# Kernel tuning notes

Measured on AMD Instinct MI355X. Metric: run time of the kernel, lower is better.

## Reference

```python
import jax, jax.numpy as jnp
import numpy as np

N_NODES = 100_000
N_EDGES = 1_600_000
N_GRAPHS = 64
IN_CH = 128
HID = 64
OUT_CH = 2


def setup_inputs() -> dict:
    key = jax.random.key(0)
    ks = jax.random.split(key, 12)

    def lin(k, fan_in, fan_out):
        s = 1.0 / np.sqrt(fan_in)
        return jax.random.uniform(k, (fan_in, fan_out), jnp.float32, -s, s)

    x = jax.random.normal(ks[0], (N_NODES, IN_CH), jnp.float32)
    edge_index = jax.random.randint(ks[1], (2, N_EDGES), 0, N_NODES, jnp.int64)
    batch = jnp.sort(jax.random.randint(ks[2], (N_NODES,), 0, N_GRAPHS, jnp.int64))
    return {
        "x": x,
        "edge_index": edge_index,
        "batch": batch,
        "w_rel0": lin(ks[3], IN_CH, HID),
        "b_rel0": jnp.zeros((HID,), jnp.float32),
        "w_root0": lin(ks[4], IN_CH, HID),
        "w_rel1": lin(ks[5], HID, HID),
        "b_rel1": jnp.zeros((HID,), jnp.float32),
        "w_root1": lin(ks[6], HID, HID),
        "w_rel2": lin(ks[7], HID, HID),
        "b_rel2": jnp.zeros((HID,), jnp.float32),
        "w_root2": lin(ks[8], HID, HID),
        "head_w1": lin(ks[9], HID, HID),
        "head_b1": jnp.zeros((HID,), jnp.float32),
        "head_w2": lin(ks[10], HID, OUT_CH),
        "head_b2": jnp.zeros((OUT_CH,), jnp.float32),
    }


def _graph_conv(x, src, dst, w_rel, b_rel, w_root):
    # PyG GraphConv: out = lin_rel(sum_{j->i} x_j) + lin_root(x_i)
    agg = jax.ops.segment_sum(x[src], dst, num_segments=N_NODES)  # [N, d_in]
    return agg @ w_rel + b_rel + x @ w_root


def reference(x, edge_index, batch, w_rel0, b_rel0, w_root0,
              w_rel1, b_rel1, w_root1, w_rel2, b_rel2, w_root2,
              head_w1, head_b1, head_w2, head_b2):
    src, dst = edge_index[0], edge_index[1]
    h = jax.nn.relu(_graph_conv(x, src, dst, w_rel0, b_rel0, w_root0))
    h = jax.nn.relu(_graph_conv(h, src, dst, w_rel1, b_rel1, w_root1))
    h = jax.nn.relu(_graph_conv(h, src, dst, w_rel2, b_rel2, w_root2))
    # global_mean_pool over graph ids (dropout is identity at inference)
    sums = jax.ops.segment_sum(h, batch, num_segments=N_GRAPHS)          # [G, H]
    cnts = jax.ops.segment_sum(jnp.ones((N_NODES,), h.dtype), batch,
                               num_segments=N_GRAPHS)                    # [G]
    pooled = sums / jnp.maximum(cnts, 1.0)[:, None]
    z = jax.nn.relu(pooled @ head_w1 + head_b1)
    return z @ head_w2 + head_b2
```

## Files before the change

### kernel.cpp

```cpp
#include <hip/hip_runtime.h>
#include <hip/hip_bf16.h>

#define CAP 64
#define KBUCK 391
#define BSHIFT 8
#define BCAP 4608
#define CHUNK_A 2048
#define AITER (CHUNK_A / 256)
#define ASTR 40
#define LDSZ (2 * 128 * ASTR * 2)

typedef __attribute__((ext_vector_type(8))) short short8;
typedef __attribute__((ext_vector_type(4))) float f32x4;

__device__ inline unsigned short bfbits(float f) {
    __hip_bfloat16 b = __float2bfloat16(f);
    unsigned short u;
    __builtin_memcpy(&u, &b, 2);
    return u;
}

__device__ inline uint4 pack8(float4 v0, float4 v1) {
    union { uint4 q; unsigned short s[8]; } pk;
    pk.s[0] = bfbits(v0.x); pk.s[1] = bfbits(v0.y);
    pk.s[2] = bfbits(v0.z); pk.s[3] = bfbits(v0.w);
    pk.s[4] = bfbits(v1.x); pk.s[5] = bfbits(v1.y);
    pk.s[6] = bfbits(v1.z); pk.s[7] = bfbits(v1.w);
    return pk.q;
}

__device__ inline void bucket_body(char* smem, int bb, const int* __restrict__ ei,
                                   int E, int* __restrict__ gcur,
                                   unsigned* __restrict__ bucketed)
{
    int* hist = (int*)smem;
    int* base = hist + KBUCK;
    const int e0 = bb * CHUNK_A;
    const int e1 = min(e0 + CHUNK_A, E);
    for (int i = threadIdx.x; i < KBUCK; i += 256) hist[i] = 0;
    __syncthreads();
    int dreg[AITER];
    #pragma unroll
    for (int it = 0; it < AITER; ++it) {
        int e = e0 + it * 256 + threadIdx.x;
        dreg[it] = (e < e1) ? ei[E + e] : -1;
        if (dreg[it] >= 0) atomicAdd(&hist[dreg[it] >> BSHIFT], 1);
    }
    __syncthreads();
    for (int i = threadIdx.x; i < KBUCK; i += 256) {
        int h = hist[i];
        base[i] = h ? atomicAdd(&gcur[i], h) : 0;
        hist[i] = 0;
    }
    __syncthreads();
    #pragma unroll
    for (int it = 0; it < AITER; ++it) {
        int e = e0 + it * 256 + threadIdx.x;
        if (e < e1) {
            int s = ei[e];
            int d = dreg[it];
            int b = d >> BSHIFT;
            int off = base[b] + atomicAdd(&hist[b], 1);
            if (off < BCAP)
                bucketed[(size_t)b * BCAP + off] = ((unsigned)s << 8) | (unsigned)(d & 255);
        }
    }
}

__global__ __launch_bounds__(256) void build_slots_kernel(
    const unsigned* __restrict__ bucketed, const int* __restrict__ gcur,
    int* __restrict__ cnt, int* __restrict__ slots, int N)
{
    __shared__ int lcnt[256];
    const int b = blockIdx.x;
    const int nb0 = b << BSHIFT;
    lcnt[threadIdx.x] = 0;
    __syncthreads();
    const int count = min(gcur[b], BCAP);
    const unsigned* src = bucketed + (size_t)b * BCAP;
    for (int i = threadIdx.x; i < count; i += 256) {
        unsigned p = src[i];
        int dl = (int)(p & 255u);
        int pos = atomicAdd(&lcnt[dl], 1);
        if (pos < CAP) slots[(size_t)(nb0 + dl) * CAP + pos] = (int)(p >> 8);
    }
    __syncthreads();
    int node = nb0 + threadIdx.x;
    if (node < N) cnt[node] = min(lcnt[threadIdx.x], CAP);
}

__global__ __launch_bounds__(256) void prep_weights_kernel(
    const float* __restrict__ wr0, const float* __restrict__ wt0,
    const float* __restrict__ wr1, const float* __restrict__ wt1,
    const float* __restrict__ wr2, const float* __restrict__ wt2,
    __hip_bfloat16* __restrict__ hi, __hip_bfloat16* __restrict__ lo,
    int* __restrict__ gcur, float* __restrict__ gsum, int* __restrict__ gcnt)
{
    int idx = blockIdx.x * 256 + threadIdx.x;
    if (idx < KBUCK) gcur[idx] = 0;
    if (idx < 64 * 64) gsum[idx] = 0.f;
    if (idx < 64) gcnt[idx] = 0;
    if (idx >= 32768) return;
    const float *wr, *wt;
    int n, k;
    if (idx < 16384)      { wr = wr0; wt = wt0; int r = idx;         n = r >> 7; k = r & 127; }
    else if (idx < 24576) { wr = wr1; wt = wt1; int r = idx - 16384; n = r >> 6; k = r & 63; }
    else                  { wr = wr2; wt = wt2; int r = idx - 24576; n = r >> 6; k = r & 63; }
    float w = (n < 64) ? wr[k * 64 + n] : wt[k * 64 + (n - 64)];
    __hip_bfloat16 h = __float2bfloat16(w);
    hi[idx] = h;
    lo[idx] = __float2bfloat16(w - __bfloat162float(h));
}

__device__ inline void store_cd(f32x4 (&acc)[4][4], int node0, int wm, int wn,
                                int kgrp, int lrow, const float* __restrict__ b_rel,
                                __hip_bfloat16* __restrict__ y,
                                __hip_bfloat16* __restrict__ r, int N)
{
    #pragma unroll
    for (int i = 0; i < 4; ++i) {
        int mbase = node0 + wm * 64 + i * 16 + kgrp * 4;
        #pragma unroll
        for (int j = 0; j < 4; ++j) {
            int n = wn * 64 + j * 16 + lrow;
            #pragma unroll
            for (int v = 0; v < 4; ++v) {
                int m = mbase + v;
                if (m < N) {
                    float val = acc[i][j][v];
                    if (n < 64) y[(size_t)m * 64 + n] = __float2bfloat16(val);
                    else        r[(size_t)m * 64 + (n - 64)] = __float2bfloat16(val + b_rel[n - 64]);
                }
            }
        }
    }
}

__device__ inline void mfma_l0_body(char* smem, int bx, const float* __restrict__ x,
    const __hip_bfloat16* __restrict__ whiT, const __hip_bfloat16* __restrict__ wloT,
    const float* __restrict__ b_rel,
    __hip_bfloat16* __restrict__ y, __hip_bfloat16* __restrict__ r, int N)
{
    __hip_bfloat16* As = (__hip_bfloat16*)smem;
    const int t = threadIdx.x;
    const int lane = t & 63;
    const int wid = t >> 6;
    const int wm = wid >> 1, wn = wid & 1;
    const int node0 = bx * 128;
    const int lrow = lane & 15;
    const int kgrp = lane >> 4;

    int sm[2], sk[2];
    const float* sp[2];
    #pragma unroll
    for (int p = 0; p < 2; ++p) {
        int c = t + p * 256;
        sm[p] = c >> 2;
        sk[p] = (c & 3) * 8;
        int row = node0 + sm[p]; if (row >= N) row = N - 1;
        sp[p] = x + (size_t)row * 128 + sk[p];
    }

    f32x4 acc[4][4];
    #pragma unroll
    for (int i = 0; i < 4; ++i)
        #pragma unroll
        for (int j = 0; j < 4; ++j) acc[i][j] = (f32x4){0.f, 0.f, 0.f, 0.f};

    #pragma unroll
    for (int p = 0; p < 2; ++p) {
        float4 v0 = *(const float4*)(sp[p]);
        float4 v1 = *(const float4*)(sp[p] + 4);
        *(uint4*)&As[sm[p] * ASTR + sk[p]] = pack8(v0, v1);
    }
    __syncthreads();

    #pragma unroll
    for (int ks = 0; ks < 4; ++ks) {
        const int buf  = (ks & 1) * (128 * ASTR);
        const int nbuf = ((ks + 1) & 1) * (128 * ASTR);

        float4 nv0[2], nv1[2];
        if (ks < 3) {
            #pragma unroll
            for (int p = 0; p < 2; ++p) {
                nv0[p] = *(const float4*)(sp[p] + (ks + 1) * 32);
                nv1[p] = *(const float4*)(sp[p] + (ks + 1) * 32 + 4);
            }
        }

        short8 a[4], bh[4], bl[4];
        #pragma unroll
        for (int i = 0; i < 4; ++i)
            a[i] = *(const short8*)&As[buf + (wm * 64 + i * 16 + lrow) * ASTR + kgrp * 8];
        #pragma unroll
        for (int j = 0; j < 4; ++j) {
            int n = wn * 64 + j * 16 + lrow;
            bh[j] = *(const short8*)(whiT + (size_t)n * 128 + ks * 32 + kgrp * 8);
            bl[j] = *(const short8*)(wloT + (size_t)n * 128 + ks * 32 + kgrp * 8);
        }
        #pragma unroll
        for (int i = 0; i < 4; ++i)
            #pragma unroll
            for (int j = 0; j < 4; ++j) {
                acc[i][j] = __builtin_amdgcn_mfma_f32_16x16x32_bf16(a[i], bh[j], acc[i][j], 0, 0, 0);
                acc[i][j] = __builtin_amdgcn_mfma_f32_16x16x32_bf16(a[i], bl[j], acc[i][j], 0, 0, 0);
            }

        if (ks < 3) {
            #pragma unroll
            for (int p = 0; p < 2; ++p)
                *(uint4*)&As[nbuf + sm[p] * ASTR + sk[p]] = pack8(nv0[p], nv1[p]);
        }
        __syncthreads();
    }

    store_cd(acc, node0, wm, wn, kgrp, lrow, b_rel, y, r, N);
}

__global__ __launch_bounds__(256) void fused_l0_kernel(
    const float* __restrict__ x,
    const __hip_bfloat16* __restrict__ whiT, const __hip_bfloat16* __restrict__ wloT,
    const float* __restrict__ b_rel,
    __hip_bfloat16* __restrict__ y, __hip_bfloat16* __restrict__ r, int N,
    int gemm_blocks, const int* __restrict__ ei, int E,
    int* __restrict__ gcur, unsigned* __restrict__ bucketed)
{
    extern __shared__ char smem[];
    if ((int)blockIdx.x < gemm_blocks)
        mfma_l0_body(smem, blockIdx.x, x, whiT, wloT, b_rel, y, r, N);
    else
        bucket_body(smem, blockIdx.x - gemm_blocks, ei, E, gcur, bucketed);
}

template <int DIN>
__global__ __launch_bounds__(256) void mfma_lin_kernel(
    const __hip_bfloat16* __restrict__ feat,
    const __hip_bfloat16* __restrict__ whiT, const __hip_bfloat16* __restrict__ wloT,
    const float* __restrict__ b_rel,
    __hip_bfloat16* __restrict__ y, __hip_bfloat16* __restrict__ r, int N)
{
    const int t = threadIdx.x;
    const int lane = t & 63;
    const int wid = t >> 6;
    const int wm = wid >> 1, wn = wid & 1;
    const int node0 = blockIdx.x * 128;
    const int lrow = lane & 15;
    const int kgrp = lane >> 4;

    f32x4 acc[4][4];
    #pragma unroll
    for (int i = 0; i < 4; ++i)
        #pragma unroll
        for (int j = 0; j < 4; ++j) acc[i][j] = (f32x4){0.f, 0.f, 0.f, 0.f};

    #pragma unroll
    for (int ks = 0; ks < DIN / 32; ++ks) {
        short8 a[4], bh[4], bl[4];
        #pragma unroll
        for (int i = 0; i < 4; ++i) {
            int row = node0 + wm * 64 + i * 16 + lrow;
            if (row >= N) row = N - 1;
            a[i] = *(const short8*)(feat + (size_t)row * DIN + ks * 32 + kgrp * 8);
        }
        #pragma unroll
        for (int j = 0; j < 4; ++j) {
            int n = wn * 64 + j * 16 + lrow;
            bh[j] = *(const short8*)(whiT + (size_t)n * DIN + ks * 32 + kgrp * 8);
            bl[j] = *(const short8*)(wloT + (size_t)n * DIN + ks * 32 + kgrp * 8);
        }
        #pragma unroll
        for (int i = 0; i < 4; ++i)
            #pragma unroll
            for (int j = 0; j < 4; ++j) {
                acc[i][j] = __builtin_amdgcn_mfma_f32_16x16x32_bf16(a[i], bh[j], acc[i][j], 0, 0, 0);
                acc[i][j] = __builtin_amdgcn_mfma_f32_16x16x32_bf16(a[i], bl[j], acc[i][j], 0, 0, 0);
            }
    }

    store_cd(acc, node0, wm, wn, kgrp, lrow, b_rel, y, r, N);
}

__global__ __launch_bounds__(256) void gather_relu_kernel(
    const __hip_bfloat16* __restrict__ y, const int* __restrict__ cnt,
    const int* __restrict__ slots, const __hip_bfloat16* __restrict__ rin,
    __hip_bfloat16* __restrict__ hout, int N)
{
    const int node = blockIdx.x * 8 + (threadIdx.x >> 5);
    if (node >= N) return;
    const int sub = threadIdx.x & 31;
    const int nb = sub >> 3;
    const int ch = (sub & 7) * 8;
    const int deg = cnt[node];
    const int* sl = slots + (size_t)node * CAP;
    const unsigned short* yp = (const unsigned short*)y;

    float a[8], b[8];
    #pragma unroll
    for (int k = 0; k < 8; ++k) { a[k] = 0.f; b[k] = 0.f; }

    #pragma unroll 2
    for (int j = nb; j < deg; j += 8) {
        int n0 = sl[j];
        uint4 v = *(const uint4*)(yp + (size_t)n0 * 64 + ch);
        a[0] += __uint_as_float(v.x << 16); a[1] += __uint_as_float(v.x & 0xffff0000u);
        a[2] += __uint_as_float(v.y << 16); a[3] += __uint_as_float(v.y & 0xffff0000u);
        a[4] += __uint_as_float(v.z << 16); a[5] += __uint_as_float(v.z & 0xffff0000u);
        a[6] += __uint_as_float(v.w << 16); a[7] += __uint_as_float(v.w & 0xffff0000u);
        int j2 = j + 4;
        if (j2 < deg) {
            int n1 = sl[j2];
            uint4 w = *(const uint4*)(yp + (size_t)n1 * 64 + ch);
            b[0] += __uint_as_float(w.x << 16); b[1] += __uint_as_float(w.x & 0xffff0000u);
            b[2] += __uint_as_float(w.y << 16); b[3] += __uint_as_float(w.y & 0xffff0000u);
            b[4] += __uint_as_float(w.z << 16); b[5] += __uint_as_float(w.z & 0xffff0000u);
            b[6] += __uint_as_float(w.w << 16); b[7] += __uint_as_float(w.w & 0xffff0000u);
        }
    }
    #pragma unroll
    for (int k = 0; k < 8; ++k) {
        a[k] += b[k];
        a[k] += __shfl_xor(a[k], 8);
        a[k] += __shfl_xor(a[k], 16);
    }
    if (nb == 0) {
        uint4 rv = *(const uint4*)((const unsigned short*)rin + (size_t)node * 64 + ch);
        float r0 = __uint_as_float(rv.x << 16), r1 = __uint_as_float(rv.x & 0xffff0000u);
        float r2 = __uint_as_float(rv.y << 16), r3 = __uint_as_float(rv.y & 0xffff0000u);
        float r4 = __uint_as_float(rv.z << 16), r5 = __uint_as_float(rv.z & 0xffff0000u);
        float r6 = __uint_as_float(rv.w << 16), r7 = __uint_as_float(rv.w & 0xffff0000u);
        float f0 = fmaxf(r0 + a[0], 0.f), f1 = fmaxf(r1 + a[1], 0.f);
        float f2 = fmaxf(r2 + a[2], 0.f), f3 = fmaxf(r3 + a[3], 0.f);
        float f4 = fmaxf(r4 + a[4], 0.f), f5 = fmaxf(r5 + a[5], 0.f);
        float f6 = fmaxf(r6 + a[6], 0.f), f7 = fmaxf(r7 + a[7], 0.f);
        union { uint4 q; unsigned short s[8]; } pk;
        pk.s[0] = bfbits(f0); pk.s[1] = bfbits(f1); pk.s[2] = bfbits(f2); pk.s[3] = bfbits(f3);
        pk.s[4] = bfbits(f4); pk.s[5] = bfbits(f5); pk.s[6] = bfbits(f6); pk.s[7] = bfbits(f7);
        *(uint4*)((unsigned short*)hout + (size_t)node * 64 + ch) = pk.q;
    }
}

__global__ __launch_bounds__(256) void pool_kernel(
    const __hip_bfloat16* __restrict__ h, const int* __restrict__ batch,
    float* __restrict__ gsum, int* __restrict__ gcnt, int N)
{
    const int CHUNK = 64;
    int wid = (blockIdx.x * 256 + threadIdx.x) >> 6;
    int lane = threadIdx.x & 63;
    int nb = lane >> 3;
    int ch = (lane & 7) * 8;
    int start = wid * CHUNK;
    if (start >= N) return;
    int end = min(start + CHUNK, N);
    const unsigned short* hp = (const unsigned short*)h;

    float a[8];
    #pragma unroll
    for (int k = 0; k < 8; ++k) a[k] = 0.f;
    int runcnt = 0;
    int i = start;
    int gcur = batch[start];

    while (i < end) {
        int idx = i + lane; if (idx > end - 1) idx = end - 1;
        int bl = batch[idx];
        unsigned long long diff = __ballot(bl != gcur && (i + lane) < end);
        int len = diff ? ((int)__ffsll(diff) - 1) : min(64, end - i);
        for (int j = i + nb; j < i + len; j += 8) {
            uint4 v = *(const uint4*)(hp + (size_t)j * 64 + ch);
            a[0] += __uint_as_float(v.x << 16); a[1] += __uint_as_float(v.x & 0xffff0000u);
            a[2] += __uint_as_float(v.y << 16); a[3] += __uint_as_float(v.y & 0xffff0000u);
            a[4] += __uint_as_float(v.z << 16); a[5] += __uint_as_float(v.z & 0xffff0000u);
            a[6] += __uint_as_float(v.w << 16); a[7] += __uint_as_float(v.w & 0xffff0000u);
        }
        runcnt += len;
        i += len;
        if (diff) {
            #pragma unroll
            for (int k = 0; k < 8; ++k) {
                a[k] += __shfl_xor(a[k], 8);
                a[k] += __shfl_xor(a[k], 16);
                a[k] += __shfl_xor(a[k], 32);
            }
            if (runcnt > 0) {
                if (nb == 0) {
                    #pragma unroll
                    for (int k = 0; k < 8; ++k)
                        atomicAdd(&gsum[gcur * 64 + ch + k], a[k]);
                }
                if (lane == 0) atomicAdd(&gcnt[gcur], runcnt);
            }
            #pragma unroll
            for (int k = 0; k < 8; ++k) a[k] = 0.f;
            runcnt = 0;
            gcur = __shfl(bl, len);
        }
    }
    #pragma unroll
    for (int k = 0; k < 8; ++k) {
        a[k] += __shfl_xor(a[k], 8);
        a[k] += __shfl_xor(a[k], 16);
        a[k] += __shfl_xor(a[k], 32);
    }
    if (runcnt > 0) {
        if (nb == 0) {
            #pragma unroll
            for (int k = 0; k < 8; ++k)
                atomicAdd(&gsum[gcur * 64 + ch + k], a[k]);
        }
        if (lane == 0) atomicAdd(&gcnt[gcur], runcnt);
    }
}

__global__ __launch_bounds__(256) void head_kernel(
    const float* __restrict__ gsum, const int* __restrict__ gcnt,
    const float* __restrict__ w1, const float* __restrict__ b1,
    const float* __restrict__ w2, const float* __restrict__ b2,
    float* __restrict__ out)
{
    __shared__ float pm[64 * 64];
    __shared__ float z[64 * 64];
    int t = threadIdx.x;
    for (int i = t; i < 64 * 64; i += 256) {
        int g = i >> 6;
        float cf = (float)gcnt[g];
        if (cf < 1.f) cf = 1.f;
        pm[i] = gsum[i] / cf;
    }
    __syncthreads();
    for (int i = t; i < 64 * 64; i += 256) {
        int g = i >> 6, c = i & 63;
        float a = b1[c];
        #pragma unroll 8
        for (int k = 0; k < 64; ++k) a = fmaf(pm[g * 64 + k], w1[k * 64 + c], a);
        z[i] = fmaxf(a, 0.f);
    }
    __syncthreads();
    for (int i = t; i < 64 * 2; i += 256) {
        int g = i >> 1, o = i & 1;
        float a = b2[o];
        #pragma unroll 8
        for (int k = 0; k < 64; ++k) a = fmaf(z[g * 64 + k], w2[k * 2 + o], a);
        out[i] = a;
    }
}

extern "C" void kernel_launch(void* const* d_in, const int* in_sizes, int n_in,
                              void* d_out, int out_size, void* d_ws, size_t ws_size,
                              hipStream_t stream)
{
    const float* x       = (const float*)d_in[0];
    const int*   ei      = (const int*)d_in[1];
    const int*   batch   = (const int*)d_in[2];
    const float* w_rel0  = (const float*)d_in[3];
    const float* b_rel0  = (const float*)d_in[4];
    const float* w_root0 = (const float*)d_in[5];
    const float* w_rel1  = (const float*)d_in[6];
    const float* b_rel1  = (const float*)d_in[7];
    const float* w_root1 = (const float*)d_in[8];
    const float* w_rel2  = (const float*)d_in[9];
    const float* b_rel2  = (const float*)d_in[10];
    const float* w_root2 = (const float*)d_in[11];
    const float* hw1     = (const float*)d_in[12];
    const float* hb1     = (const float*)d_in[13];
    const float* hw2     = (const float*)d_in[14];
    const float* hb2     = (const float*)d_in[15];
    float* out = (float*)d_out;

    const int N = in_sizes[0] / 128;
    const int E = in_sizes[1] / 2;
    const int G = 64;

    size_t off = 0;
    auto alloc = [&](size_t bytes) -> void* {
        void* p = (char*)d_ws + off;
        off += (bytes + 255) & ~(size_t)255;
        return p;
    };
    int*      cnt      = (int*)alloc((size_t)N * 4);
    int*      slots    = (int*)alloc((size_t)N * CAP * 4);
    unsigned* bucketed = (unsigned*)alloc((size_t)KBUCK * BCAP * 4);
    int*      gcur     = (int*)alloc((size_t)KBUCK * 4);
    __hip_bfloat16* whiT = (__hip_bfloat16*)alloc(32768 * 2);
    __hip_bfloat16* wloT = (__hip_bfloat16*)alloc(32768 * 2);
    __hip_bfloat16* ybf  = (__hip_bfloat16*)alloc((size_t)N * 64 * 2);
    __hip_bfloat16* h0   = (__hip_bfloat16*)alloc((size_t)N * 64 * 2);
    __hip_bfloat16* h1   = (__hip_bfloat16*)alloc((size_t)N * 64 * 2);
    __hip_bfloat16* rbf  = (__hip_bfloat16*)alloc((size_t)N * 64 * 2);
    float* gsum     = (float*)alloc((size_t)G * 64 * 4);
    int*   gcnt     = (int*)alloc((size_t)G * 4);
    (void)ws_size; (void)n_in;

    prep_weights_kernel<<<128, 256, 0, stream>>>(w_rel0, w_root0, w_rel1, w_root1,
                                                 w_rel2, w_root2, whiT, wloT,
                                                 gcur, gsum, gcnt);

    const int gemm_blocks = (N + 127) / 128;
    const int bucket_blocks = (E + CHUNK_A - 1) / CHUNK_A;
    const int gather_blocks = (N + 7) / 8;

    fused_l0_kernel<<<gemm_blocks + bucket_blocks, 256, LDSZ, stream>>>(
        x, whiT, wloT, b_rel0, ybf, rbf, N, gemm_blocks, ei, E, gcur, bucketed);
    build_slots_kernel<<<KBUCK, 256, 0, stream>>>(bucketed, gcur, cnt, slots, N);
    gather_relu_kernel<<<gather_blocks, 256, 0, stream>>>(ybf, cnt, slots, rbf, h0, N);

    mfma_lin_kernel<64><<<gemm_blocks, 256, 0, stream>>>(
        h0, whiT + 16384, wloT + 16384, b_rel1, ybf, rbf, N);
    gather_relu_kernel<<<gather_blocks, 256, 0, stream>>>(ybf, cnt, slots, rbf, h1, N);

    mfma_lin_kernel<64><<<gemm_blocks, 256, 0, stream>>>(
        h1, whiT + 24576, wloT + 24576, b_rel2, ybf, rbf, N);
    gather_relu_kernel<<<gather_blocks, 256, 0, stream>>>(ybf, cnt, slots, rbf, h0, N);

    int pool_waves  = (N + 63) / 64;
    int pool_blocks = (pool_waves + 3) / 4;
    pool_kernel<<<pool_blocks, 256, 0, stream>>>(h0, batch, gsum, gcnt, N);
    head_kernel<<<1, 256, 0, stream>>>(gsum, gcnt, hw1, hb1, hw2, hb2, out);
}
```

Before: 391.0 us.

## Fuse mean-pool into last gather, pad bucket counters, enlarge bucketing chunks

```diff
diff --git a/kernel.cpp b/kernel.cpp
--- a/kernel.cpp
+++ b/kernel.cpp
@@ -5,8 +5,9 @@
 #define KBUCK 391
 #define BSHIFT 8
 #define BCAP 4608
-#define CHUNK_A 2048
+#define CHUNK_A 8192
 #define AITER (CHUNK_A / 256)
+#define GPAD 16
 #define ASTR 40
 #define LDSZ (2 * 128 * ASTR * 2)
 
@@ -39,26 +40,24 @@
     const int e1 = min(e0 + CHUNK_A, E);
     for (int i = threadIdx.x; i < KBUCK; i += 256) hist[i] = 0;
     __syncthreads();
-    int dreg[AITER];
-    #pragma unroll
+    #pragma unroll 4
     for (int it = 0; it < AITER; ++it) {
         int e = e0 + it * 256 + threadIdx.x;
-        dreg[it] = (e < e1) ? ei[E + e] : -1;
-        if (dreg[it] >= 0) atomicAdd(&hist[dreg[it] >> BSHIFT], 1);
+        if (e < e1) atomicAdd(&hist[ei[E + e] >> BSHIFT], 1);
     }
     __syncthreads();
     for (int i = threadIdx.x; i < KBUCK; i += 256) {
         int h = hist[i];
-        base[i] = h ? atomicAdd(&gcur[i], h) : 0;
+        base[i] = h ? atomicAdd(&gcur[i * GPAD], h) : 0;
         hist[i] = 0;
     }
     __syncthreads();
-    #pragma unroll
+    #pragma unroll 4
     for (int it = 0; it < AITER; ++it) {
         int e = e0 + it * 256 + threadIdx.x;
         if (e < e1) {
             int s = ei[e];
-            int d = dreg[it];
+            int d = ei[E + e];
             int b = d >> BSHIFT;
             int off = base[b] + atomicAdd(&hist[b], 1);
             if (off < BCAP)
@@ -76,7 +75,7 @@
     const int nb0 = b << BSHIFT;
     lcnt[threadIdx.x] = 0;
     __syncthreads();
-    const int count = min(gcur[b], BCAP);
+    const int count = min(gcur[b * GPAD], BCAP);
     const unsigned* src = bucketed + (size_t)b * BCAP;
     for (int i = threadIdx.x; i < count; i += 256) {
         unsigned p = src[i];
@@ -97,7 +96,7 @@
     int* __restrict__ gcur, float* __restrict__ gsum, int* __restrict__ gcnt)
 {
     int idx = blockIdx.x * 256 + threadIdx.x;
-    if (idx < KBUCK) gcur[idx] = 0;
+    if (idx < KBUCK * GPAD) gcur[idx] = 0;
     if (idx < 64 * 64) gsum[idx] = 0.f;
     if (idx < 64) gcnt[idx] = 0;
     if (idx >= 32768) return;
@@ -189,16 +188,18 @@
             }
         }
 
-        short8 a[4], bh[4], bl[4];
-        #pragma unroll
-        for (int i = 0; i < 4; ++i)
-            a[i] = *(const short8*)&As[buf + (wm * 64 + i * 16 + lrow) * ASTR + kgrp * 8];
+        short8 bh[4], bl[4];
         #pragma unroll
         for (int j = 0; j < 4; ++j) {
             int n = wn * 64 + j * 16 + lrow;
             bh[j] = *(const short8*)(whiT + (size_t)n * 128 + ks * 32 + kgrp * 8);
             bl[j] = *(const short8*)(wloT + (size_t)n * 128 + ks * 32 + kgrp * 8);
         }
+        short8 a[4];
+        #pragma unroll
+        for (int i = 0; i < 4; ++i)
+            a[i] = *(const short8*)&As[buf + (wm * 64 + i * 16 + lrow) * ASTR + kgrp * 8];
+
         #pragma unroll
         for (int i = 0; i < 4; ++i)
             #pragma unroll
@@ -223,14 +224,14 @@
     const __hip_bfloat16* __restrict__ whiT, const __hip_bfloat16* __restrict__ wloT,
     const float* __restrict__ b_rel,
     __hip_bfloat16* __restrict__ y, __hip_bfloat16* __restrict__ r, int N,
-    int gemm_blocks, const int* __restrict__ ei, int E,
+    int bucket_blocks, const int* __restrict__ ei, int E,
     int* __restrict__ gcur, unsigned* __restrict__ bucketed)
 {
     extern __shared__ char smem[];
-    if ((int)blockIdx.x < gemm_blocks)
-        mfma_l0_body(smem, blockIdx.x, x, whiT, wloT, b_rel, y, r, N);
+    if ((int)blockIdx.x < bucket_blocks)
+        bucket_body(smem, blockIdx.x, ei, E, gcur, bucketed);
     else
-        bucket_body(smem, blockIdx.x - gemm_blocks, ei, E, gcur, bucketed);
+        mfma_l0_body(smem, blockIdx.x - bucket_blocks, x, whiT, wloT, b_rel, y, r, N);
 }
 
 template <int DIN>
@@ -281,19 +282,27 @@
     store_cd(acc, node0, wm, wn, kgrp, lrow, b_rel, y, r, N);
 }
 
+template <int POOL>
 __global__ __launch_bounds__(256) void gather_relu_kernel(
     const __hip_bfloat16* __restrict__ y, const int* __restrict__ cnt,
     const int* __restrict__ slots, const __hip_bfloat16* __restrict__ rin,
-    __hip_bfloat16* __restrict__ hout, int N)
-{
-    const int node = blockIdx.x * 8 + (threadIdx.x >> 5);
-    if (node >= N) return;
+    __hip_bfloat16* __restrict__ hout,
+    const int* __restrict__ batch, float* __restrict__ gsum,
+    int* __restrict__ gcnt, int N)
+{
+    __shared__ float hl[8][64];
+    __shared__ int gl[8];
+    const int grp = threadIdx.x >> 5;
+    const int node = blockIdx.x * 8 + grp;
+    const bool active = node < N;
     const int sub = threadIdx.x & 31;
     const int nb = sub >> 3;
     const int ch = (sub & 7) * 8;
-    const int deg = cnt[node];
+    const int deg = active ? cnt[node] : 0;
     const int* sl = slots + (size_t)node * CAP;
     const unsigned short* yp = (const unsigned short*)y;
+
+    if (POOL && sub == 0) gl[grp] = active ? batch[node] : -1;
 
     float a[8], b[8];
     #pragma unroll
@@ -324,91 +333,58 @@
         a[k] += __shfl_xor(a[k], 16);
     }
     if (nb == 0) {
-        uint4 rv = *(const uint4*)((const unsigned short*)rin + (size_t)node * 64 + ch);
-        float r0 = __uint_as_float(rv.x << 16), r1 = __uint_as_float(rv.x & 0xffff0000u);
-        float r2 = __uint_as_float(rv.y << 16), r3 = __uint_as_float(rv.y & 0xffff0000u);
-        float r4 = __uint_as_float(rv.z << 16), r5 = __uint_as_float(rv.z & 0xffff0000u);
-        float r6 = __uint_as_float(rv.w << 16), r7 = __uint_as_float(rv.w & 0xffff0000u);
-        float f0 = fmaxf(r0 + a[0], 0.f), f1 = fmaxf(r1 + a[1], 0.f);
-        float f2 = fmaxf(r2 + a[2], 0.f), f3 = fmaxf(r3 + a[3], 0.f);
-        float f4 = fmaxf(r4 + a[4], 0.f), f5 = fmaxf(r5 + a[5], 0.f);
-        float f6 = fmaxf(r6 + a[6], 0.f), f7 = fmaxf(r7 + a[7], 0.f);
-        union { uint4 q; unsigned short s[8]; } pk;
-        pk.s[0] = bfbits(f0); pk.s[1] = bfbits(f1); pk.s[2] = bfbits(f2); pk.s[3] = bfbits(f3);
-        pk.s[4] = bfbits(f4); pk.s[5] = bfbits(f5); pk.s[6] = bfbits(f6); pk.s[7] = bfbits(f7);
-        *(uint4*)((unsigned short*)hout + (size_t)node * 64 + ch) = pk.q;
-    }
-}
-
-__global__ __launch_bounds__(256) void pool_kernel(
-    const __hip_bfloat16* __restrict__ h, const int* __restrict__ batch,
-    float* __restrict__ gsum, int* __restrict__ gcnt, int N)
-{
-    const int CHUNK = 64;
-    int wid = (blockIdx.x * 256 + threadIdx.x) >> 6;
-    int lane = threadIdx.x & 63;
-    int nb = lane >> 3;
-    int ch = (lane & 7) * 8;
-    int start = wid * CHUNK;
-    if (start >= N) return;
-    int end = min(start + CHUNK, N);
-    const unsigned short* hp = (const unsigned short*)h;
-
-    float a[8];
-    #pragma unroll
-    for (int k = 0; k < 8; ++k) a[k] = 0.f;
-    int runcnt = 0;
-    int i = start;
-    int gcur = batch[start];
-
-    while (i < end) {
-        int idx = i + lane; if (idx > end - 1) idx = end - 1;
-        int bl = batch[idx];
-        unsigned long long diff = __ballot(bl != gcur && (i + lane) < end);
-        int len = diff ? ((int)__ffsll(diff) - 1) : min(64, end - i);
-        for (int j = i + nb; j < i + len; j += 8) {
-            uint4 v = *(const uint4*)(hp + (size_t)j * 64 + ch);
-            a[0] += __uint_as_float(v.x << 16); a[1] += __uint_as_float(v.x & 0xffff0000u);
-            a[2] += __uint_as_float(v.y << 16); a[3] += __uint_as_float(v.y & 0xffff0000u);
-            a[4] += __uint_as_float(v.z << 16); a[5] += __uint_as_float(v.z & 0xffff0000u);
-            a[6] += __uint_as_float(v.w << 16); a[7] += __uint_as_float(v.w & 0xffff0000u);
-        }
-        runcnt += len;
-        i += len;
-        if (diff) {
-            #pragma unroll
-            for (int k = 0; k < 8; ++k) {
-                a[k] += __shfl_xor(a[k], 8);
-                a[k] += __shfl_xor(a[k], 16);
-                a[k] += __shfl_xor(a[k], 32);
-            }
-            if (runcnt > 0) {
-                if (nb == 0) {
-                    #pragma unroll
-                    for (int k = 0; k < 8; ++k)
-                        atomicAdd(&gsum[gcur * 64 + ch + k], a[k]);
+        float f[8];
+        if (active) {
+            uint4 rv = *(const uint4*)((const unsigned short*)rin + (size_t)node * 64 + ch);
+            float r0 = __uint_as_float(rv.x << 16), r1 = __uint_as_float(rv.x & 0xffff0000u);
+            float r2 = __uint_as_float(rv.y << 16), r3 = __uint_as_float(rv.y & 0xffff0000u);
+            float r4 = __uint_as_float(rv.z << 16), r5 = __uint_as_float(rv.z & 0xffff0000u);
+            float r6 = __uint_as_float(rv.w << 16), r7 = __uint_as_float(rv.w & 0xffff0000u);
+            f[0] = fmaxf(r0 + a[0], 0.f); f[1] = fmaxf(r1 + a[1], 0.f);
+            f[2] = fmaxf(r2 + a[2], 0.f); f[3] = fmaxf(r3 + a[3], 0.f);
+            f[4] = fmaxf(r4 + a[4], 0.f); f[5] = fmaxf(r5 + a[5], 0.f);
+            f[6] = fmaxf(r6 + a[6], 0.f); f[7] = fmaxf(r7 + a[7], 0.f);
+        } else {
+            #pragma unroll
+            for (int k = 0; k < 8; ++k) f[k] = 0.f;
+        }
+        if (POOL) {
+            #pragma unroll
+            for (int k = 0; k < 8; ++k)
+                hl[grp][ch + k] = __uint_as_float((unsigned)bfbits(f[k]) << 16);
+        } else if (active) {
+            union { uint4 q; unsigned short s[8]; } pk;
+            #pragma unroll
+            for (int k = 0; k < 8; ++k) pk.s[k] = bfbits(f[k]);
+            *(uint4*)((unsigned short*)hout + (size_t)node * 64 + ch) = pk.q;
+        }
+    }
+    if (POOL) {
+        __syncthreads();
+        int t = threadIdx.x;
+        if (t < 64) {
+            float acc = 0.f; int g = gl[0];
+            #pragma unroll
+            for (int i = 0; i < 8; ++i) {
+                if (gl[i] != g) {
+                    if (g >= 0) atomicAdd(&gsum[g * 64 + t], acc);
+                    acc = 0.f; g = gl[i];
                 }
-                if (lane == 0) atomicAdd(&gcnt[gcur], runcnt);
-            }
-            #pragma unroll
-            for (int k = 0; k < 8; ++k) a[k] = 0.f;
-            runcnt = 0;
-            gcur = __shfl(bl, len);
-        }
-    }
-    #pragma unroll
-    for (int k = 0; k < 8; ++k) {
-        a[k] += __shfl_xor(a[k], 8);
-        a[k] += __shfl_xor(a[k], 16);
-        a[k] += __shfl_xor(a[k], 32);
-    }
-    if (runcnt > 0) {
-        if (nb == 0) {
-            #pragma unroll
-            for (int k = 0; k < 8; ++k)
-                atomicAdd(&gsum[gcur * 64 + ch + k], a[k]);
-        }
-        if (lane == 0) atomicAdd(&gcnt[gcur], runcnt);
+                acc += hl[i][t];
+            }
+            if (g >= 0) atomicAdd(&gsum[g * 64 + t], acc);
+        } else if (t == 64) {
+            int c = 0; int g = gl[0];
+            #pragma unroll
+            for (int i = 0; i < 8; ++i) {
+                if (gl[i] != g) {
+                    if (g >= 0) atomicAdd(&gcnt[g], c);
+                    c = 0; g = gl[i];
+                }
+                if (gl[i] >= 0) c++;
+            }
+            if (g >= 0) atomicAdd(&gcnt[g], c);
+        }
     }
 }
 
@@ -480,7 +456,7 @@
     int*      cnt      = (int*)alloc((size_t)N * 4);
     int*      slots    = (int*)alloc((size_t)N * CAP * 4);
     unsigned* bucketed = (unsigned*)alloc((size_t)KBUCK * BCAP * 4);
-    int*      gcur     = (int*)alloc((size_t)KBUCK * 4);
+    int*      gcur     = (int*)alloc((size_t)KBUCK * GPAD * 4);
     __hip_bfloat16* whiT = (__hip_bfloat16*)alloc(32768 * 2);
     __hip_bfloat16* wloT = (__hip_bfloat16*)alloc(32768 * 2);
     __hip_bfloat16* ybf  = (__hip_bfloat16*)alloc((size_t)N * 64 * 2);
@@ -499,21 +475,21 @@
     const int bucket_blocks = (E + CHUNK_A - 1) / CHUNK_A;
     const int gather_blocks = (N + 7) / 8;
 
-    fused_l0_kernel<<<gemm_blocks + bucket_blocks, 256, LDSZ, stream>>>(
-        x, whiT, wloT, b_rel0, ybf, rbf, N, gemm_blocks, ei, E, gcur, bucketed);
+    fused_l0_kernel<<<bucket_blocks + gemm_blocks, 256, LDSZ, stream>>>(
+        x, whiT, wloT, b_rel0, ybf, rbf, N, bucket_blocks, ei, E, gcur, bucketed);
     build_slots_kernel<<<KBUCK, 256, 0, stream>>>(bucketed, gcur, cnt, slots, N);
-    gather_relu_kernel<<<gather_blocks, 256, 0, stream>>>(ybf, cnt, slots, rbf, h0, N);
+    gather_relu_kernel<0><<<gather_blocks, 256, 0, stream>>>(
+        ybf, cnt, slots, rbf, h0, nullptr, nullptr, nullptr, N);
 
     mfma_lin_kernel<64><<<gemm_blocks, 256, 0, stream>>>(
         h0, whiT + 16384, wloT + 16384, b_rel1, ybf, rbf, N);
-    gather_relu_kernel<<<gather_blocks, 256, 0, stream>>>(ybf, cnt, slots, rbf, h1, N);
+    gather_relu_kernel<0><<<gather_blocks, 256, 0, stream>>>(
+        ybf, cnt, slots, rbf, h1, nullptr, nullptr, nullptr, N);
 
     mfma_lin_kernel<64><<<gemm_blocks, 256, 0, stream>>>(
         h1, whiT + 24576, wloT + 24576, b_rel2, ybf, rbf, N);
-    gather_relu_kernel<<<gather_blocks, 256, 0, stream>>>(ybf, cnt, slots, rbf, h0, N);
-
-    int pool_waves  = (N + 63) / 64;
-    int pool_blocks = (pool_waves + 3) / 4;
-    pool_kernel<<<pool_blocks, 256, 0, stream>>>(h0, batch, gsum, gcnt, N);
+    gather_relu_kernel<1><<<gather_blocks, 256, 0, stream>>>(
+        ybf, cnt, slots, rbf, nullptr, batch, gsum, gcnt, N);
+
     head_kernel<<<1, 256, 0, stream>>>(gsum, gcnt, hw1, hb1, hw2, hb2, out);
 }
```

After: 454.1 us. +16.1%, slower.
